# Kernel optimization log

Measured on AMD Instinct MI355X. Metric: run time of the kernel, lower is better.

## Reference

```python
import jax, jax.numpy as jnp
import numpy as np

NUM_CLASSES = 80
ALPHA = 0.25
GAMMA = 2.0
CONF_T = 0.5
IOU_T = 0.5
N_ANCHORS = 6144


def _pairwise_iou(b):
    # b: [n,4] (x1,y1,x2,y2) -> [n,n] IoU matrix
    area = (b[:, 2] - b[:, 0]) * (b[:, 3] - b[:, 1])
    lt = jnp.maximum(b[:, None, :2], b[None, :, :2])
    rb = jnp.minimum(b[:, None, 2:], b[None, :, 2:])
    wh = jnp.clip(rb - lt, 0.0)
    inter = wh[..., 0] * wh[..., 1]
    return inter / (area[:, None] + area[None, :] - inter)


def _nms(boxes, scores, thr):
    # torchvision-style NMS: returns kept indices in decreasing-score order
    order = jnp.argsort(-scores)
    iou = _pairwise_iou(boxes[order])
    n = boxes.shape[0]
    ar = jnp.arange(n)
    def body(i, supp):
        return supp | ((iou[i] > thr) & (ar > i) & jnp.logical_not(supp[i]))
    supp = jax.lax.fori_loop(0, n, body, jnp.zeros(n, dtype=bool))
    kept_pos = jnp.where(~supp)[0]  # eager: concrete shapes
    return order[kept_pos]


def _make_boxes(tb, floc):
    # tb: [1,1,4] target box; floc: [Nf,2] filtered predicted locations
    # replicates loc_determined with T=1: (tx1*px, ty1*py, tx2*px, ty2*py)
    px, py = floc[:, 0], floc[:, 1]
    return jnp.stack([tb[0, 0, 0] * px, tb[0, 0, 1] * py,
                      tb[0, 0, 2] * px, tb[0, 0, 3] * py], axis=1)


def _smooth_l1_sum(pred, tgt):
    d = jnp.abs(pred - tgt)  # broadcasts [k,C,4] vs [1,1,4]
    return jnp.where(d < 1.0, 0.5 * d * d, d - 0.5).sum()


def setup_inputs() -> dict:
    key = jax.random.key(0)
    k1, k2, k3 = jax.random.split(key, 3)
    locations = jax.random.uniform(k1, (1, N_ANCHORS, 2), dtype=jnp.float32)
    confidences = jax.random.uniform(k2, (1, N_ANCHORS, NUM_CLASSES), dtype=jnp.float32)
    # valid target box (x1<x2, y1<y2) in [0,1]
    target_boxes = jnp.array([[[0.15, 0.2, 0.85, 0.9]]], dtype=jnp.float32)
    target_labels = jax.random.randint(k3, (1,), 0, NUM_CLASSES)
    return {"locations": locations, "confidences": confidences,
            "target_boxes": target_boxes, "target_labels": target_labels}


def reference(locations, confidences, target_boxes, target_labels):
    conf = confidences[0]                       # [N,C]
    scores_max = conf.max(axis=1)
    idx_f = jnp.where(scores_max > CONF_T)[0]   # eager boolean filter
    if idx_f.shape[0] == 0:
        return jnp.float32(0.001)
    floc = locations[0, idx_f, :]               # [Nf,2]
    fconf = conf[idx_f]                         # [Nf,C]
    boxes = _make_boxes(target_boxes, floc)     # [Nf,4] (pred_loc_final)
    score = fconf[:, 0]                         # class-0 score, as in original
    keep = _nms(boxes, score, IOU_T)            # kept indices
    if keep.shape[0] == 0:
        return jnp.float32(0.001)
    matched_loc = boxes[keep]                   # [M,4]
    matched_conf = fconf[keep]                  # [M,C]
    k = target_labels.shape[0]                  # = 1
    topv, topi = jax.lax.top_k(matched_conf.T, k)  # per-class top-k over dim 0
    topv, topi = topv.T, topi.T                 # [k,C]
    pred_bin = (topv[:, 0] > 0.5).astype(jnp.float32)  # [k]
    mloc = matched_loc[topi]                    # [k,C,4]
    loc_loss = _smooth_l1_sum(mloc, target_boxes)
    # F.cross_entropy with 1-D float input/target = probabilities mode, unbatched
    ce = -(target_labels.astype(jnp.float32) * jax.nn.log_softmax(pred_bin)).sum()
    focal = ALPHA * (1.0 - jnp.exp(-ce)) ** GAMMA * ce
    # original bug preserved: num_positives = sum of kept *indices*
    num_pos = keep.sum().astype(jnp.float32)
    return (loc_loss + focal) / num_pos
```

## Files before the change

kernel.cpp:

```cpp
#include <hip/hip_runtime.h>
#include <stdint.h>

#define N_ANCHORS 6144
#define NUM_CLASSES 80
#define NWORDS 96

__device__ unsigned long long g_mask[(size_t)N_ANCHORS * NWORDS];
__device__ float4 g_boxes[N_ANCHORS];
__device__ float4 g_sbox[N_ANCHORS];
__device__ float  g_key[N_ANCHORS];
__device__ int    g_rank[N_ANCHORS];
__device__ int    g_fic[N_ANCHORS];
__device__ int    g_sAnchor[N_ANCHORS];
__device__ int    g_sFi[N_ANCHORS];
__device__ int    g_keptPos[N_ANCHORS];
__device__ int    g_F, g_K, g_np;
__device__ float  g_loss;

__device__ __forceinline__ unsigned long long shfl64(unsigned long long v, int l) {
    return __shfl(v, l, 64);
}

__global__ void k_zero() {
    int i = blockIdx.x * 256 + threadIdx.x;
    if (i < N_ANCHORS) { g_rank[i] = 0; g_fic[i] = 0; }
    if (i == 0) { g_F = 0; g_K = 0; g_np = 0; g_loss = 0.0f; }
}

__global__ void k_prep(const float* __restrict__ loc, const float* __restrict__ conf,
                       const float* __restrict__ tb) {
    int i = blockIdx.x * 256 + threadIdx.x;
    if (i >= N_ANCHORS) return;
    const float4* cp4 = (const float4*)(conf + (size_t)i * NUM_CLASSES);
    float4 v0 = cp4[0];
    float score = v0.x;
    float m = fmaxf(fmaxf(v0.x, v0.y), fmaxf(v0.z, v0.w));
    #pragma unroll
    for (int c = 1; c < NUM_CLASSES / 4; ++c) {
        float4 v = cp4[c];
        m = fmaxf(m, fmaxf(fmaxf(v.x, v.y), fmaxf(v.z, v.w)));
    }
    bool valid = m > 0.5f;
    g_key[i] = valid ? score : -1.0f;
    float px = loc[2 * i], py = loc[2 * i + 1];
    float4 b;
    b.x = __fmul_rn(tb[0], px);
    b.y = __fmul_rn(tb[1], py);
    b.z = __fmul_rn(tb[2], px);
    b.w = __fmul_rn(tb[3], py);
    g_boxes[i] = b;
    if (valid) atomicAdd(&g_F, 1);
}

__global__ void k_rank(void) {
    __shared__ float skey[256];
    int j0 = blockIdx.y * 256;
    skey[threadIdx.x] = g_key[j0 + threadIdx.x];
    __syncthreads();
    int i = blockIdx.x * 256 + threadIdx.x;
    float ki = g_key[i];
    int r = 0, f = 0;
    #pragma unroll 8
    for (int jj = 0; jj < 256; ++jj) {
        float kj = skey[jj];
        int j = j0 + jj;
        bool valid_j = kj >= 0.0f;
        r += (kj > ki) || (kj == ki && j < i && valid_j);
        f += (j < i) && valid_j;
    }
    atomicAdd(&g_rank[i], r);
    atomicAdd(&g_fic[i], f);
}

__global__ void k_scatter(void) {
    int i = blockIdx.x * 256 + threadIdx.x;
    if (i >= N_ANCHORS) return;
    if (g_key[i] >= 0.0f) {
        int p = g_rank[i];
        g_sAnchor[p] = i;
        g_sFi[p] = g_fic[i];
        g_sbox[p] = g_boxes[i];
    }
}

__global__ void __launch_bounds__(256) k_mask(void) {
    int wave = (blockIdx.x * 256 + threadIdx.x) >> 6;
    int lane = threadIdx.x & 63;
    if (wave >= N_ANCHORS) return;
    int i = wave;
    float4 bi = g_sbox[i];
    float areai = __fmul_rn(bi.z - bi.x, bi.w - bi.y);
    unsigned long long* row = g_mask + (size_t)i * NWORDS;
    for (int w = (i >> 6); w < NWORDS; ++w) {
        float4 bj = g_sbox[w * 64 + lane];
        float areaj = __fmul_rn(bj.z - bj.x, bj.w - bj.y);
        float lx = fmaxf(bi.x, bj.x), ly = fmaxf(bi.y, bj.y);
        float rx = fminf(bi.z, bj.z), ry = fminf(bi.w, bj.w);
        float iw = fmaxf(rx - lx, 0.0f), ih = fmaxf(ry - ly, 0.0f);
        float inter = __fmul_rn(iw, ih);
        float denom = __fsub_rn(__fadd_rn(areai, areaj), inter);
        float iou = __fdiv_rn(inter, denom);
        unsigned long long bits = __ballot(iou > 0.5f);
        if (lane == 0) row[w] = bits;
    }
}

__global__ void __launch_bounds__(64) k_scan(void) {
    int lane = threadIdx.x;
    int F = g_F;
    auto initw = [&](int w) -> unsigned long long {
        long long lo = (long long)w * 64, hi = lo + 64;
        if (F <= lo) return ~0ull;
        if (F >= hi) return 0ull;
        return (~0ull) << (F - lo);
    };
    unsigned long long remv0 = initw(lane);
    unsigned long long remv1 = (lane < 32) ? initw(64 + lane) : ~0ull;
    unsigned long long kept0 = 0, kept1 = 0;

    for (int w = 0; w < NWORDS; ++w) {
        unsigned long long cur = (w < 64) ? shfl64(remv0, w) : shfl64(remv1, w - 64);
        unsigned long long cand = ~cur;
        while (cand) {
            unsigned long long tmp = cand;
            int pos[8];
            #pragma unroll
            for (int q = 0; q < 8; ++q) {
                pos[q] = tmp ? __builtin_ctzll(tmp) : 64;
                tmp &= tmp - 1;
            }
            unsigned long long r0[8], r1[8];
            #pragma unroll
            for (int q = 0; q < 8; ++q) {
                if (pos[q] < 64) {
                    const unsigned long long* row = g_mask + (size_t)(w * 64 + pos[q]) * NWORDS;
                    r0[q] = row[lane];
                    r1[q] = (lane < 32) ? row[64 + lane] : 0ull;
                } else { r0[q] = 0ull; r1[q] = 0ull; }
            }
            unsigned long long m = cur, keptloc = 0, batch = 0;
            #pragma unroll
            for (int q = 0; q < 8; ++q) {
                if (pos[q] < 64) {
                    batch |= 1ull << pos[q];
                    if (!((m >> pos[q]) & 1ull)) {
                        keptloc |= 1ull << pos[q];
                        unsigned long long iw = (w < 64) ? shfl64(r0[q], w) : shfl64(r1[q], w - 64);
                        m |= iw;
                    }
                }
            }
            #pragma unroll
            for (int q = 0; q < 8; ++q)
                if ((pos[q] < 64) && ((keptloc >> pos[q]) & 1ull)) { remv0 |= r0[q]; remv1 |= r1[q]; }
            if (w < 64) { if (lane == w) kept0 |= keptloc; }
            else        { if (lane == w - 64) kept1 |= keptloc; }
            cur = m;
            cand = cand & ~batch & ~m;
        }
    }

    int c0 = __popcll(kept0);
    int c1 = (lane < 32) ? __popcll(kept1) : 0;
    int x0 = c0, x1 = c1;
    for (int ofs = 1; ofs < 64; ofs <<= 1) {
        int y0 = __shfl_up(x0, ofs, 64);
        int y1 = __shfl_up(x1, ofs, 64);
        if (lane >= ofs) { x0 += y0; x1 += y1; }
    }
    int t0 = __shfl(x0, 63, 64);
    int t1 = __shfl(x1, 63, 64);
    int off = x0 - c0;
    unsigned long long wd = kept0;
    while (wd) { int b = __builtin_ctzll(wd); g_keptPos[off++] = lane * 64 + b; wd &= wd - 1; }
    off = t0 + (x1 - c1);
    wd = kept1;
    while (wd) { int b = __builtin_ctzll(wd); g_keptPos[off++] = (64 + lane) * 64 + b; wd &= wd - 1; }
    if (lane == 0) g_K = t0 + t1;
}

__global__ void __launch_bounds__(64) k_loss(const float* __restrict__ conf, const float* __restrict__ tb) {
    int c = blockIdx.x;
    int lane = threadIdx.x;
    int K = g_K;
    float bv = -3.402823466e+38f;
    int bk = 0x7fffffff;
    int np = 0;
    for (int k = lane; k < K; k += 64) {
        int p = g_keptPos[k];
        int a = g_sAnchor[p];
        float v = conf[(size_t)a * NUM_CLASSES + c];
        if (v > bv || (v == bv && k < bk)) { bv = v; bk = k; }
        if (c == 0) np += g_sFi[p];
    }
    for (int ofs = 32; ofs > 0; ofs >>= 1) {
        float ov = __shfl_down(bv, ofs, 64);
        int ok = __shfl_down(bk, ofs, 64);
        if (ov > bv || (ov == bv && ok < bk)) { bv = ov; bk = ok; }
    }
    if (c == 0) {
        for (int ofs = 32; ofs > 0; ofs >>= 1) np += __shfl_down(np, ofs, 64);
        if (lane == 0) g_np = np;
    }
    if (lane == 0 && K > 0) {
        float4 b = g_sbox[g_keptPos[bk]];
        float t0 = tb[0], t1 = tb[1], t2 = tb[2], t3 = tb[3];
        float l = 0.0f, d;
        d = fabsf(b.x - t0); l += (d < 1.0f) ? 0.5f * d * d : d - 0.5f;
        d = fabsf(b.y - t1); l += (d < 1.0f) ? 0.5f * d * d : d - 0.5f;
        d = fabsf(b.z - t2); l += (d < 1.0f) ? 0.5f * d * d : d - 0.5f;
        d = fabsf(b.w - t3); l += (d < 1.0f) ? 0.5f * d * d : d - 0.5f;
        atomicAdd(&g_loss, l);
    }
}

__global__ void k_final(float* __restrict__ out) {
    out[0] = (g_F == 0 || g_K == 0) ? 0.001f : g_loss / (float)g_np;
}

extern "C" void kernel_launch(void* const* d_in, const int* in_sizes, int n_in,
                              void* d_out, int out_size, void* d_ws, size_t ws_size,
                              hipStream_t stream) {
    const float* loc  = (const float*)d_in[0];
    const float* conf = (const float*)d_in[1];
    const float* tb   = (const float*)d_in[2];
    float* out = (float*)d_out;

    k_zero<<<24, 256, 0, stream>>>();
    k_prep<<<24, 256, 0, stream>>>(loc, conf, tb);
    k_rank<<<dim3(24, 24), 256, 0, stream>>>();
    k_scatter<<<24, 256, 0, stream>>>();
    k_mask<<<(N_ANCHORS * 64) / 256, 256, 0, stream>>>();
    k_scan<<<1, 64, 0, stream>>>();
    k_loss<<<NUM_CLASSES, 64, 0, stream>>>(conf, tb);
    k_final<<<1, 1, 0, stream>>>(out);
}
```

Measured before the change: 182.5 us.

## Prefetch NMS mask rows across words, drop atomics and fuse loss finalization

The serial NMS scan now prefetches up to 12 candidate mask rows for the next word while it resolves the current one, so global-load latency overlaps the dependent suppression chain. Leftover candidates are handled in a slow path. Atomic rank accumulation and the zero kernel are replaced by per-tile partial arrays that the scatter kernel sums. Prep uses four threads per anchor, and the loss and final kernels merge into one 1024-thread block that reduces through shared memory. The cost is more registers in the single-wave scan and wasted loads when prefetched rows turn out to be suppressed.

New measurement: 249.8 us. 36.9% more time.

```diff
diff --git a/kernel.cpp b/kernel.cpp
--- a/kernel.cpp
+++ b/kernel.cpp
@@ -4,55 +4,54 @@
 #define N_ANCHORS 6144
 #define NUM_CLASSES 80
 #define NWORDS 96
+#define JT 24
+#define NP 12
 
 __device__ unsigned long long g_mask[(size_t)N_ANCHORS * NWORDS];
 __device__ float4 g_boxes[N_ANCHORS];
 __device__ float4 g_sbox[N_ANCHORS];
 __device__ float  g_key[N_ANCHORS];
-__device__ int    g_rank[N_ANCHORS];
-__device__ int    g_fic[N_ANCHORS];
+__device__ int    g_rankP[JT][N_ANCHORS];
+__device__ int    g_ficP[JT][N_ANCHORS];
+__device__ int    g_vcnt[JT];
 __device__ int    g_sAnchor[N_ANCHORS];
 __device__ int    g_sFi[N_ANCHORS];
 __device__ int    g_keptPos[N_ANCHORS];
-__device__ int    g_F, g_K, g_np;
-__device__ float  g_loss;
+__device__ int    g_F, g_K;
 
 __device__ __forceinline__ unsigned long long shfl64(unsigned long long v, int l) {
     return __shfl(v, l, 64);
 }
 
-__global__ void k_zero() {
-    int i = blockIdx.x * 256 + threadIdx.x;
-    if (i < N_ANCHORS) { g_rank[i] = 0; g_fic[i] = 0; }
-    if (i == 0) { g_F = 0; g_K = 0; g_np = 0; g_loss = 0.0f; }
-}
-
-__global__ void k_prep(const float* __restrict__ loc, const float* __restrict__ conf,
-                       const float* __restrict__ tb) {
-    int i = blockIdx.x * 256 + threadIdx.x;
-    if (i >= N_ANCHORS) return;
-    const float4* cp4 = (const float4*)(conf + (size_t)i * NUM_CLASSES);
+__global__ void __launch_bounds__(256) k_prep(const float* __restrict__ loc,
+                                              const float* __restrict__ conf,
+                                              const float* __restrict__ tb) {
+    int tid = blockIdx.x * 256 + threadIdx.x;
+    int a = tid >> 2, q = tid & 3;
+    const float4* cp4 = (const float4*)(conf + (size_t)a * NUM_CLASSES) + q * 5;
     float4 v0 = cp4[0];
-    float score = v0.x;
     float m = fmaxf(fmaxf(v0.x, v0.y), fmaxf(v0.z, v0.w));
     #pragma unroll
-    for (int c = 1; c < NUM_CLASSES / 4; ++c) {
+    for (int c = 1; c < 5; ++c) {
         float4 v = cp4[c];
         m = fmaxf(m, fmaxf(fmaxf(v.x, v.y), fmaxf(v.z, v.w)));
     }
-    bool valid = m > 0.5f;
-    g_key[i] = valid ? score : -1.0f;
-    float px = loc[2 * i], py = loc[2 * i + 1];
-    float4 b;
-    b.x = __fmul_rn(tb[0], px);
-    b.y = __fmul_rn(tb[1], py);
-    b.z = __fmul_rn(tb[2], px);
-    b.w = __fmul_rn(tb[3], py);
-    g_boxes[i] = b;
-    if (valid) atomicAdd(&g_F, 1);
-}
-
-__global__ void k_rank(void) {
+    m = fmaxf(m, __shfl_xor(m, 1, 64));
+    m = fmaxf(m, __shfl_xor(m, 2, 64));
+    if (q == 0) {
+        bool valid = m > 0.5f;
+        g_key[a] = valid ? v0.x : -1.0f;
+        float2 p = ((const float2*)loc)[a];
+        float4 b;
+        b.x = __fmul_rn(tb[0], p.x);
+        b.y = __fmul_rn(tb[1], p.y);
+        b.z = __fmul_rn(tb[2], p.x);
+        b.w = __fmul_rn(tb[3], p.y);
+        g_boxes[a] = b;
+    }
+}
+
+__global__ void __launch_bounds__(256) k_rank(void) {
     __shared__ float skey[256];
     int j0 = blockIdx.y * 256;
     skey[threadIdx.x] = g_key[j0 + threadIdx.x];
@@ -68,18 +67,31 @@
         r += (kj > ki) || (kj == ki && j < i && valid_j);
         f += (j < i) && valid_j;
     }
-    atomicAdd(&g_rank[i], r);
-    atomicAdd(&g_fic[i], f);
-}
-
-__global__ void k_scatter(void) {
+    g_rankP[blockIdx.y][i] = r;
+    g_ficP[blockIdx.y][i] = f;
+    if (blockIdx.x == 0 && threadIdx.x == 0) {
+        int c = 0;
+        for (int jj = 0; jj < 256; ++jj) c += (skey[jj] >= 0.0f);
+        g_vcnt[blockIdx.y] = c;
+    }
+}
+
+__global__ void __launch_bounds__(256) k_scatter(void) {
     int i = blockIdx.x * 256 + threadIdx.x;
+    if (i == 0) {
+        int F = 0;
+        #pragma unroll
+        for (int j = 0; j < JT; ++j) F += g_vcnt[j];
+        g_F = F;
+    }
     if (i >= N_ANCHORS) return;
     if (g_key[i] >= 0.0f) {
-        int p = g_rank[i];
-        g_sAnchor[p] = i;
-        g_sFi[p] = g_fic[i];
-        g_sbox[p] = g_boxes[i];
+        int r = 0, f = 0;
+        #pragma unroll
+        for (int j = 0; j < JT; ++j) { r += g_rankP[j][i]; f += g_ficP[j][i]; }
+        g_sAnchor[r] = i;
+        g_sFi[r] = f;
+        g_sbox[r] = g_boxes[i];
     }
 }
 
@@ -118,46 +130,65 @@
     unsigned long long remv1 = (lane < 32) ? initw(64 + lane) : ~0ull;
     unsigned long long kept0 = 0, kept1 = 0;
 
-    for (int w = 0; w < NWORDS; ++w) {
+    int ppA[NP], ppB[NP];
+    unsigned long long pA0[NP], pA1[NP], pB0[NP], pB1[NP];
+
+    auto prefetch = [&](int word, int* pp, unsigned long long* p0, unsigned long long* p1) {
+        unsigned long long cur = (word < 64) ? shfl64(remv0, word) : shfl64(remv1, word - 64);
+        unsigned long long cand = ~cur;
+        #pragma unroll
+        for (int q = 0; q < NP; ++q) {
+            int pos = cand ? __builtin_ctzll(cand) : 64;
+            cand &= cand - 1;
+            pp[q] = pos;
+            if (pos < 64) {
+                const unsigned long long* row = g_mask + (size_t)(word * 64 + pos) * NWORDS;
+                p0[q] = row[lane];
+                p1[q] = (lane < 32) ? row[64 + lane] : 0ull;
+            } else { p0[q] = 0ull; p1[q] = 0ull; }
+        }
+    };
+
+    auto resolve = [&](int w, const int* pp, const unsigned long long* p0, const unsigned long long* p1) {
         unsigned long long cur = (w < 64) ? shfl64(remv0, w) : shfl64(remv1, w - 64);
-        unsigned long long cand = ~cur;
-        while (cand) {
-            unsigned long long tmp = cand;
-            int pos[8];
-            #pragma unroll
-            for (int q = 0; q < 8; ++q) {
-                pos[q] = tmp ? __builtin_ctzll(tmp) : 64;
-                tmp &= tmp - 1;
+        unsigned long long m = cur, keptloc = 0;
+        #pragma unroll
+        for (int q = 0; q < NP; ++q) {
+            int pos = pp[q];
+            if (pos < 64 && !((m >> pos) & 1ull)) {
+                keptloc |= 1ull << pos;
+                unsigned long long iw = (w < 64) ? shfl64(p0[q], w) : shfl64(p1[q], w - 64);
+                m |= iw;
+                remv0 |= p0[q];
+                remv1 |= p1[q];
             }
-            unsigned long long r0[8], r1[8];
-            #pragma unroll
-            for (int q = 0; q < 8; ++q) {
-                if (pos[q] < 64) {
-                    const unsigned long long* row = g_mask + (size_t)(w * 64 + pos[q]) * NWORDS;
-                    r0[q] = row[lane];
-                    r1[q] = (lane < 32) ? row[64 + lane] : 0ull;
-                } else { r0[q] = 0ull; r1[q] = 0ull; }
-            }
-            unsigned long long m = cur, keptloc = 0, batch = 0;
-            #pragma unroll
-            for (int q = 0; q < 8; ++q) {
-                if (pos[q] < 64) {
-                    batch |= 1ull << pos[q];
-                    if (!((m >> pos[q]) & 1ull)) {
-                        keptloc |= 1ull << pos[q];
-                        unsigned long long iw = (w < 64) ? shfl64(r0[q], w) : shfl64(r1[q], w - 64);
-                        m |= iw;
-                    }
-                }
-            }
-            #pragma unroll
-            for (int q = 0; q < 8; ++q)
-                if ((pos[q] < 64) && ((keptloc >> pos[q]) & 1ull)) { remv0 |= r0[q]; remv1 |= r1[q]; }
-            if (w < 64) { if (lane == w) kept0 |= keptloc; }
-            else        { if (lane == w - 64) kept1 |= keptloc; }
-            cur = m;
-            cand = cand & ~batch & ~m;
-        }
+        }
+        int last = pp[NP - 1];
+        unsigned long long leftover = (last >= 63) ? 0ull : ((~m) & ((~0ull) << (last + 1)));
+        while (leftover) {
+            int pos = __builtin_ctzll(leftover);
+            leftover &= leftover - 1;
+            if ((m >> pos) & 1ull) continue;
+            const unsigned long long* row = g_mask + (size_t)(w * 64 + pos) * NWORDS;
+            unsigned long long r0 = row[lane];
+            unsigned long long r1 = (lane < 32) ? row[64 + lane] : 0ull;
+            keptloc |= 1ull << pos;
+            unsigned long long iw = (w < 64) ? shfl64(r0, w) : shfl64(r1, w - 64);
+            m |= iw;
+            remv0 |= r0;
+            remv1 |= r1;
+            leftover &= ~m;
+        }
+        if (w < 64) { if (lane == w) kept0 |= keptloc; }
+        else        { if (lane == w - 64) kept1 |= keptloc; }
+    };
+
+    prefetch(0, ppA, pA0, pA1);
+    for (int w = 0; w < NWORDS; w += 2) {
+        if (w + 1 < NWORDS) prefetch(w + 1, ppB, pB0, pB1);
+        resolve(w, ppA, pA0, pA1);
+        if (w + 2 < NWORDS) prefetch(w + 2, ppA, pA0, pA1);
+        if (w + 1 < NWORDS) resolve(w + 1, ppB, pB0, pB1);
     }
 
     int c0 = __popcll(kept0);
@@ -179,43 +210,54 @@
     if (lane == 0) g_K = t0 + t1;
 }
 
-__global__ void __launch_bounds__(64) k_loss(const float* __restrict__ conf, const float* __restrict__ tb) {
-    int c = blockIdx.x;
-    int lane = threadIdx.x;
+__global__ void __launch_bounds__(1024) k_loss(const float* __restrict__ conf,
+                                               const float* __restrict__ tb,
+                                               float* __restrict__ out) {
+    __shared__ float sloss[NUM_CLASSES];
+    __shared__ int snp;
+    int wave = threadIdx.x >> 6, lane = threadIdx.x & 63;
     int K = g_K;
-    float bv = -3.402823466e+38f;
-    int bk = 0x7fffffff;
-    int np = 0;
-    for (int k = lane; k < K; k += 64) {
-        int p = g_keptPos[k];
-        int a = g_sAnchor[p];
-        float v = conf[(size_t)a * NUM_CLASSES + c];
-        if (v > bv || (v == bv && k < bk)) { bv = v; bk = k; }
-        if (c == 0) np += g_sFi[p];
-    }
-    for (int ofs = 32; ofs > 0; ofs >>= 1) {
-        float ov = __shfl_down(bv, ofs, 64);
-        int ok = __shfl_down(bk, ofs, 64);
-        if (ov > bv || (ov == bv && ok < bk)) { bv = ov; bk = ok; }
-    }
-    if (c == 0) {
-        for (int ofs = 32; ofs > 0; ofs >>= 1) np += __shfl_down(np, ofs, 64);
-        if (lane == 0) g_np = np;
-    }
-    if (lane == 0 && K > 0) {
-        float4 b = g_sbox[g_keptPos[bk]];
-        float t0 = tb[0], t1 = tb[1], t2 = tb[2], t3 = tb[3];
-        float l = 0.0f, d;
-        d = fabsf(b.x - t0); l += (d < 1.0f) ? 0.5f * d * d : d - 0.5f;
-        d = fabsf(b.y - t1); l += (d < 1.0f) ? 0.5f * d * d : d - 0.5f;
-        d = fabsf(b.z - t2); l += (d < 1.0f) ? 0.5f * d * d : d - 0.5f;
-        d = fabsf(b.w - t3); l += (d < 1.0f) ? 0.5f * d * d : d - 0.5f;
-        atomicAdd(&g_loss, l);
-    }
-}
-
-__global__ void k_final(float* __restrict__ out) {
-    out[0] = (g_F == 0 || g_K == 0) ? 0.001f : g_loss / (float)g_np;
+    float t0 = tb[0], t1 = tb[1], t2 = tb[2], t3 = tb[3];
+    for (int c = wave; c < NUM_CLASSES; c += 16) {
+        float bv = -3.402823466e+38f;
+        int bk = 0x7fffffff;
+        int np = 0;
+        for (int k = lane; k < K; k += 64) {
+            int p = g_keptPos[k];
+            int a = g_sAnchor[p];
+            float v = conf[(size_t)a * NUM_CLASSES + c];
+            if (v > bv || (v == bv && k < bk)) { bv = v; bk = k; }
+            if (c == 0) np += g_sFi[p];
+        }
+        for (int ofs = 32; ofs > 0; ofs >>= 1) {
+            float ov = __shfl_down(bv, ofs, 64);
+            int ok = __shfl_down(bk, ofs, 64);
+            if (ov > bv || (ov == bv && ok < bk)) { bv = ov; bk = ok; }
+        }
+        if (c == 0) {
+            for (int ofs = 32; ofs > 0; ofs >>= 1) np += __shfl_down(np, ofs, 64);
+            if (lane == 0) snp = np;
+        }
+        if (lane == 0 && K > 0) {
+            float4 b = g_sbox[g_keptPos[bk]];
+            float l = 0.0f, d;
+            d = fabsf(b.x - t0); l += (d < 1.0f) ? 0.5f * d * d : d - 0.5f;
+            d = fabsf(b.y - t1); l += (d < 1.0f) ? 0.5f * d * d : d - 0.5f;
+            d = fabsf(b.z - t2); l += (d < 1.0f) ? 0.5f * d * d : d - 0.5f;
+            d = fabsf(b.w - t3); l += (d < 1.0f) ? 0.5f * d * d : d - 0.5f;
+            sloss[c] = l;
+        }
+    }
+    __syncthreads();
+    if (threadIdx.x == 0) {
+        if (g_F == 0 || K == 0) {
+            out[0] = 0.001f;
+        } else {
+            float l = 0.0f;
+            for (int c = 0; c < NUM_CLASSES; ++c) l += sloss[c];
+            out[0] = l / (float)snp;
+        }
+    }
 }
 
 extern "C" void kernel_launch(void* const* d_in, const int* in_sizes, int n_in,
@@ -226,12 +268,10 @@
     const float* tb   = (const float*)d_in[2];
     float* out = (float*)d_out;
 
-    k_zero<<<24, 256, 0, stream>>>();
-    k_prep<<<24, 256, 0, stream>>>(loc, conf, tb);
+    k_prep<<<96, 256, 0, stream>>>(loc, conf, tb);
     k_rank<<<dim3(24, 24), 256, 0, stream>>>();
     k_scatter<<<24, 256, 0, stream>>>();
     k_mask<<<(N_ANCHORS * 64) / 256, 256, 0, stream>>>();
     k_scan<<<1, 64, 0, stream>>>();
-    k_loss<<<NUM_CLASSES, 64, 0, stream>>>(conf, tb);
-    k_final<<<1, 1, 0, stream>>>(out);
-}
+    k_loss<<<1, 1024, 0, stream>>>(conf, tb, out);
+}
```

## Fuse NMS pipeline into one persistent kernel with grid barriers

Applied to the files above, without the earlier changes.

Replaces eight launches with a single persistent kernel of 256 blocks that uses atomic grid barriers between stages (prep, rank/scatter, IoU mask, scan, loss). Ranking is now computed per anchor by 8 cooperating threads instead of tiled atomics. The NMS scan is software-pipelined, prefetching three batches of mask rows ahead of resolving suppression. This aims to remove launch overhead and serial scan latency, but relies on all blocks being co-resident for the spin barriers.

After: 560.9 us. +207.4%, slower.

```diff
diff --git a/kernel.cpp b/kernel.cpp
--- a/kernel.cpp
+++ b/kernel.cpp
@@ -1,221 +1,278 @@
 #include <hip/hip_runtime.h>
 #include <stdint.h>
 
-#define N_ANCHORS 6144
-#define NUM_CLASSES 80
-#define NWORDS 96
-
-__device__ unsigned long long g_mask[(size_t)N_ANCHORS * NWORDS];
-__device__ float4 g_boxes[N_ANCHORS];
-__device__ float4 g_sbox[N_ANCHORS];
-__device__ float  g_key[N_ANCHORS];
-__device__ int    g_rank[N_ANCHORS];
-__device__ int    g_fic[N_ANCHORS];
-__device__ int    g_sAnchor[N_ANCHORS];
-__device__ int    g_sFi[N_ANCHORS];
-__device__ int    g_keptPos[N_ANCHORS];
-__device__ int    g_F, g_K, g_np;
-__device__ float  g_loss;
-
-__device__ __forceinline__ unsigned long long shfl64(unsigned long long v, int l) {
-    return __shfl(v, l, 64);
-}
-
-__global__ void k_zero() {
-    int i = blockIdx.x * 256 + threadIdx.x;
-    if (i < N_ANCHORS) { g_rank[i] = 0; g_fic[i] = 0; }
-    if (i == 0) { g_F = 0; g_K = 0; g_np = 0; g_loss = 0.0f; }
-}
-
-__global__ void k_prep(const float* __restrict__ loc, const float* __restrict__ conf,
-                       const float* __restrict__ tb) {
-    int i = blockIdx.x * 256 + threadIdx.x;
-    if (i >= N_ANCHORS) return;
-    const float4* cp4 = (const float4*)(conf + (size_t)i * NUM_CLASSES);
-    float4 v0 = cp4[0];
-    float score = v0.x;
-    float m = fmaxf(fmaxf(v0.x, v0.y), fmaxf(v0.z, v0.w));
-    #pragma unroll
-    for (int c = 1; c < NUM_CLASSES / 4; ++c) {
-        float4 v = cp4[c];
-        m = fmaxf(m, fmaxf(fmaxf(v.x, v.y), fmaxf(v.z, v.w)));
-    }
-    bool valid = m > 0.5f;
-    g_key[i] = valid ? score : -1.0f;
-    float px = loc[2 * i], py = loc[2 * i + 1];
-    float4 b;
-    b.x = __fmul_rn(tb[0], px);
-    b.y = __fmul_rn(tb[1], py);
-    b.z = __fmul_rn(tb[2], px);
-    b.w = __fmul_rn(tb[3], py);
-    g_boxes[i] = b;
-    if (valid) atomicAdd(&g_F, 1);
-}
-
-__global__ void k_rank(void) {
-    __shared__ float skey[256];
-    int j0 = blockIdx.y * 256;
-    skey[threadIdx.x] = g_key[j0 + threadIdx.x];
+#define NA 6144
+#define NC 80
+#define NW 96
+#define NB 256
+#define NT 256
+
+typedef unsigned long long u64;
+
+__device__ u64    g_mask[(size_t)NA * NW];
+__device__ float4 g_boxes[NA];
+__device__ float4 g_sbox[NA];
+__device__ __align__(16) float g_key[NA];
+__device__ int    g_sAnchor[NA];
+__device__ int    g_sFi[NA];
+__device__ int    g_keptPos[NA];
+
+struct Ctl { int bar[8]; int F; int K; int np; float loss; };
+__device__ Ctl g_ctl;
+
+__device__ __forceinline__ u64 shfl64(u64 v, int l) {
+    int lo = __shfl((int)(v & 0xffffffffull), l, 64);
+    int hi = __shfl((int)(v >> 32), l, 64);
+    return ((u64)(unsigned)hi << 32) | (unsigned)lo;
+}
+
+__device__ __forceinline__ void gbar(int id) {
     __syncthreads();
-    int i = blockIdx.x * 256 + threadIdx.x;
-    float ki = g_key[i];
-    int r = 0, f = 0;
-    #pragma unroll 8
-    for (int jj = 0; jj < 256; ++jj) {
-        float kj = skey[jj];
-        int j = j0 + jj;
-        bool valid_j = kj >= 0.0f;
-        r += (kj > ki) || (kj == ki && j < i && valid_j);
-        f += (j < i) && valid_j;
-    }
-    atomicAdd(&g_rank[i], r);
-    atomicAdd(&g_fic[i], f);
-}
-
-__global__ void k_scatter(void) {
-    int i = blockIdx.x * 256 + threadIdx.x;
-    if (i >= N_ANCHORS) return;
-    if (g_key[i] >= 0.0f) {
-        int p = g_rank[i];
-        g_sAnchor[p] = i;
-        g_sFi[p] = g_fic[i];
-        g_sbox[p] = g_boxes[i];
-    }
-}
-
-__global__ void __launch_bounds__(256) k_mask(void) {
-    int wave = (blockIdx.x * 256 + threadIdx.x) >> 6;
-    int lane = threadIdx.x & 63;
-    if (wave >= N_ANCHORS) return;
-    int i = wave;
-    float4 bi = g_sbox[i];
-    float areai = __fmul_rn(bi.z - bi.x, bi.w - bi.y);
-    unsigned long long* row = g_mask + (size_t)i * NWORDS;
-    for (int w = (i >> 6); w < NWORDS; ++w) {
-        float4 bj = g_sbox[w * 64 + lane];
-        float areaj = __fmul_rn(bj.z - bj.x, bj.w - bj.y);
-        float lx = fmaxf(bi.x, bj.x), ly = fmaxf(bi.y, bj.y);
-        float rx = fminf(bi.z, bj.z), ry = fminf(bi.w, bj.w);
-        float iw = fmaxf(rx - lx, 0.0f), ih = fmaxf(ry - ly, 0.0f);
-        float inter = __fmul_rn(iw, ih);
-        float denom = __fsub_rn(__fadd_rn(areai, areaj), inter);
-        float iou = __fdiv_rn(inter, denom);
-        unsigned long long bits = __ballot(iou > 0.5f);
-        if (lane == 0) row[w] = bits;
-    }
-}
-
-__global__ void __launch_bounds__(64) k_scan(void) {
-    int lane = threadIdx.x;
-    int F = g_F;
-    auto initw = [&](int w) -> unsigned long long {
-        long long lo = (long long)w * 64, hi = lo + 64;
-        if (F <= lo) return ~0ull;
-        if (F >= hi) return 0ull;
-        return (~0ull) << (F - lo);
-    };
-    unsigned long long remv0 = initw(lane);
-    unsigned long long remv1 = (lane < 32) ? initw(64 + lane) : ~0ull;
-    unsigned long long kept0 = 0, kept1 = 0;
-
-    for (int w = 0; w < NWORDS; ++w) {
-        unsigned long long cur = (w < 64) ? shfl64(remv0, w) : shfl64(remv1, w - 64);
-        unsigned long long cand = ~cur;
-        while (cand) {
-            unsigned long long tmp = cand;
-            int pos[8];
+    if (threadIdx.x == 0) {
+        __threadfence();
+        atomicAdd(&g_ctl.bar[id], 1);
+        while (__hip_atomic_load(&g_ctl.bar[id], __ATOMIC_ACQUIRE,
+                                 __HIP_MEMORY_SCOPE_AGENT) < NB)
+            __builtin_amdgcn_s_sleep(1);
+        __threadfence();
+    }
+    __syncthreads();
+}
+
+__global__ void __launch_bounds__(NT, 1)
+k_fused(const float* __restrict__ loc, const float* __restrict__ conf,
+        const float* __restrict__ tb, float* __restrict__ out) {
+    const int tid  = blockIdx.x * NT + threadIdx.x;
+    const int lane = threadIdx.x & 63;
+
+    if (tid < NA * 4) {
+        int a = tid >> 2, q = tid & 3;
+        const float4* cp4 = (const float4*)(conf + (size_t)a * NC) + q * 5;
+        float4 v0 = cp4[0];
+        float m = fmaxf(fmaxf(v0.x, v0.y), fmaxf(v0.z, v0.w));
+        #pragma unroll
+        for (int c = 1; c < 5; ++c) {
+            float4 v = cp4[c];
+            m = fmaxf(m, fmaxf(fmaxf(v.x, v.y), fmaxf(v.z, v.w)));
+        }
+        m = fmaxf(m, __shfl_xor(m, 1, 64));
+        m = fmaxf(m, __shfl_xor(m, 2, 64));
+        bool valid = m > 0.5f;
+        if (q == 0) {
+            g_key[a] = valid ? v0.x : -1.0f;
+            float2 p = ((const float2*)loc)[a];
+            float4 b;
+            b.x = __fmul_rn(tb[0], p.x);
+            b.y = __fmul_rn(tb[1], p.y);
+            b.z = __fmul_rn(tb[2], p.x);
+            b.w = __fmul_rn(tb[3], p.y);
+            g_boxes[a] = b;
+        }
+        u64 bal = __ballot(valid && q == 0);
+        if (lane == 0) atomicAdd(&g_ctl.F, (int)__popcll(bal));
+    }
+
+    gbar(0);
+
+    {
+        int a = tid >> 3, s = tid & 7;
+        if (a < NA) {
+            float ki = g_key[a];
+            const float4* k4 = (const float4*)g_key;
+            int r = 0, f = 0;
+            for (int jj = 0; jj < 192; ++jj) {
+                int i4 = jj * 8 + s;
+                float4 kj = k4[i4];
+                int j0 = i4 * 4;
+                r += (kj.x > ki) || (kj.x == ki && (j0 + 0) < a);
+                r += (kj.y > ki) || (kj.y == ki && (j0 + 1) < a);
+                r += (kj.z > ki) || (kj.z == ki && (j0 + 2) < a);
+                r += (kj.w > ki) || (kj.w == ki && (j0 + 3) < a);
+                f += ((j0 + 0) < a) && (kj.x >= 0.0f);
+                f += ((j0 + 1) < a) && (kj.y >= 0.0f);
+                f += ((j0 + 2) < a) && (kj.z >= 0.0f);
+                f += ((j0 + 3) < a) && (kj.w >= 0.0f);
+            }
+            r += __shfl_xor(r, 1, 64); r += __shfl_xor(r, 2, 64); r += __shfl_xor(r, 4, 64);
+            f += __shfl_xor(f, 1, 64); f += __shfl_xor(f, 2, 64); f += __shfl_xor(f, 4, 64);
+            if (s == 0 && ki >= 0.0f) {
+                g_sAnchor[r] = a;
+                g_sFi[r] = f;
+                g_sbox[r] = g_boxes[a];
+            }
+        }
+    }
+
+    gbar(1);
+
+    {
+        int gw = tid >> 6;
+        for (int row = gw; row < NA; row += (NB * NT) / 64) {
+            float4 bi = g_sbox[row];
+            float areai = __fmul_rn(bi.z - bi.x, bi.w - bi.y);
+            u64* rp = g_mask + (size_t)row * NW;
+            for (int w = row >> 6; w < NW; ++w) {
+                float4 bj = g_sbox[w * 64 + lane];
+                float areaj = __fmul_rn(bj.z - bj.x, bj.w - bj.y);
+                float lx = fmaxf(bi.x, bj.x), ly = fmaxf(bi.y, bj.y);
+                float rx = fminf(bi.z, bj.z), ry = fminf(bi.w, bj.w);
+                float iw = fmaxf(rx - lx, 0.0f), ih = fmaxf(ry - ly, 0.0f);
+                float inter = __fmul_rn(iw, ih);
+                float denom = __fsub_rn(__fadd_rn(areai, areaj), inter);
+                float iou = __fdiv_rn(inter, denom);
+                u64 bits = __ballot(iou > 0.5f);
+                if (lane == 0) rp[w] = bits;
+            }
+        }
+    }
+
+    gbar(2);
+
+    if (blockIdx.x == 0 && threadIdx.x < 64) {
+        int F = g_ctl.F;
+        auto initw = [&](int w) -> u64 {
+            long long lo = (long long)w * 64, hi = lo + 64;
+            if (F <= lo) return ~0ull;
+            if (F >= hi) return 0ull;
+            return (~0ull) << (F - lo);
+        };
+        u64 remv0 = initw(lane);
+        u64 remv1 = (lane < 32) ? initw(64 + lane) : ~0ull;
+        u64 kept0 = 0, kept1 = 0;
+
+        auto getRemv = [&](int w) -> u64 {
+            return (w < 64) ? shfl64(remv0, w) : shfl64(remv1, w - 64);
+        };
+
+        int scanW = 0;
+        u64 scanRem = ~getRemv(0);
+
+        int posA[8], posB[8], posC[8];
+        u64 loA[8], hiA[8], loB[8], hiB[8], loC[8], hiC[8];
+
+        auto fill = [&](int* pos, u64* lo, u64* hi) -> int {
+            scanRem &= ~getRemv(scanW);
+            int n = 0;
             #pragma unroll
             for (int q = 0; q < 8; ++q) {
-                pos[q] = tmp ? __builtin_ctzll(tmp) : 64;
-                tmp &= tmp - 1;
-            }
-            unsigned long long r0[8], r1[8];
+                while (scanRem == 0 && scanW < NW - 1) { ++scanW; scanRem = ~getRemv(scanW); }
+                int p = -1;
+                if (scanRem) {
+                    int b = __builtin_ctzll(scanRem);
+                    scanRem &= scanRem - 1;
+                    p = (scanW << 6) | b;
+                    ++n;
+                }
+                pos[q] = p;
+            }
             #pragma unroll
             for (int q = 0; q < 8; ++q) {
-                if (pos[q] < 64) {
-                    const unsigned long long* row = g_mask + (size_t)(w * 64 + pos[q]) * NWORDS;
-                    r0[q] = row[lane];
-                    r1[q] = (lane < 32) ? row[64 + lane] : 0ull;
-                } else { r0[q] = 0ull; r1[q] = 0ull; }
-            }
-            unsigned long long m = cur, keptloc = 0, batch = 0;
+                const u64* row = g_mask + (size_t)(pos[q] < 0 ? 0 : pos[q]) * NW;
+                lo[q] = row[lane];
+                hi[q] = row[64 + (lane & 31)];
+            }
+            return n;
+        };
+
+        auto resolve = [&](const int* pos, const u64* lo, const u64* hi) {
             #pragma unroll
             for (int q = 0; q < 8; ++q) {
-                if (pos[q] < 64) {
-                    batch |= 1ull << pos[q];
-                    if (!((m >> pos[q]) & 1ull)) {
-                        keptloc |= 1ull << pos[q];
-                        unsigned long long iw = (w < 64) ? shfl64(r0[q], w) : shfl64(r1[q], w - 64);
-                        m |= iw;
-                    }
+                int p = pos[q];
+                if (p < 0) break;
+                int wq = p >> 6, bq = p & 63;
+                bool ownerbit;
+                if (wq < 64) ownerbit = (lane == wq) && ((remv0 >> bq) & 1ull);
+                else         ownerbit = (lane == wq - 64) && ((remv1 >> bq) & 1ull);
+                bool suppressed = __ballot(ownerbit) != 0ull;
+                if (!suppressed) {
+                    remv0 |= lo[q];
+                    remv1 |= hi[q];
+                    if (wq < 64) { if (lane == wq) kept0 |= 1ull << bq; }
+                    else         { if (lane == wq - 64) kept1 |= 1ull << bq; }
                 }
             }
-            #pragma unroll
-            for (int q = 0; q < 8; ++q)
-                if ((pos[q] < 64) && ((keptloc >> pos[q]) & 1ull)) { remv0 |= r0[q]; remv1 |= r1[q]; }
-            if (w < 64) { if (lane == w) kept0 |= keptloc; }
-            else        { if (lane == w - 64) kept1 |= keptloc; }
-            cur = m;
-            cand = cand & ~batch & ~m;
-        }
-    }
-
-    int c0 = __popcll(kept0);
-    int c1 = (lane < 32) ? __popcll(kept1) : 0;
-    int x0 = c0, x1 = c1;
-    for (int ofs = 1; ofs < 64; ofs <<= 1) {
-        int y0 = __shfl_up(x0, ofs, 64);
-        int y1 = __shfl_up(x1, ofs, 64);
-        if (lane >= ofs) { x0 += y0; x1 += y1; }
-    }
-    int t0 = __shfl(x0, 63, 64);
-    int t1 = __shfl(x1, 63, 64);
-    int off = x0 - c0;
-    unsigned long long wd = kept0;
-    while (wd) { int b = __builtin_ctzll(wd); g_keptPos[off++] = lane * 64 + b; wd &= wd - 1; }
-    off = t0 + (x1 - c1);
-    wd = kept1;
-    while (wd) { int b = __builtin_ctzll(wd); g_keptPos[off++] = (64 + lane) * 64 + b; wd &= wd - 1; }
-    if (lane == 0) g_K = t0 + t1;
-}
-
-__global__ void __launch_bounds__(64) k_loss(const float* __restrict__ conf, const float* __restrict__ tb) {
-    int c = blockIdx.x;
-    int lane = threadIdx.x;
-    int K = g_K;
-    float bv = -3.402823466e+38f;
-    int bk = 0x7fffffff;
-    int np = 0;
-    for (int k = lane; k < K; k += 64) {
-        int p = g_keptPos[k];
-        int a = g_sAnchor[p];
-        float v = conf[(size_t)a * NUM_CLASSES + c];
-        if (v > bv || (v == bv && k < bk)) { bv = v; bk = k; }
-        if (c == 0) np += g_sFi[p];
-    }
-    for (int ofs = 32; ofs > 0; ofs >>= 1) {
-        float ov = __shfl_down(bv, ofs, 64);
-        int ok = __shfl_down(bk, ofs, 64);
-        if (ov > bv || (ov == bv && ok < bk)) { bv = ov; bk = ok; }
-    }
-    if (c == 0) {
-        for (int ofs = 32; ofs > 0; ofs >>= 1) np += __shfl_down(np, ofs, 64);
-        if (lane == 0) g_np = np;
-    }
-    if (lane == 0 && K > 0) {
-        float4 b = g_sbox[g_keptPos[bk]];
-        float t0 = tb[0], t1 = tb[1], t2 = tb[2], t3 = tb[3];
-        float l = 0.0f, d;
-        d = fabsf(b.x - t0); l += (d < 1.0f) ? 0.5f * d * d : d - 0.5f;
-        d = fabsf(b.y - t1); l += (d < 1.0f) ? 0.5f * d * d : d - 0.5f;
-        d = fabsf(b.z - t2); l += (d < 1.0f) ? 0.5f * d * d : d - 0.5f;
-        d = fabsf(b.w - t3); l += (d < 1.0f) ? 0.5f * d * d : d - 0.5f;
-        atomicAdd(&g_loss, l);
-    }
-}
-
-__global__ void k_final(float* __restrict__ out) {
-    out[0] = (g_F == 0 || g_K == 0) ? 0.001f : g_loss / (float)g_np;
+        };
+
+        int nA = fill(posA, loA, hiA);
+        if (nA) {
+            int nB = fill(posB, loB, hiB);
+            int nC;
+            for (;;) {
+                nC = fill(posC, loC, hiC);
+                resolve(posA, loA, hiA);
+                if (nB == 0) break;
+                nA = fill(posA, loA, hiA);
+                resolve(posB, loB, hiB);
+                if (nC == 0) break;
+                nB = fill(posB, loB, hiB);
+                resolve(posC, loC, hiC);
+                if (nA == 0) break;
+            }
+        }
+
+        int c0 = __popcll(kept0);
+        int c1 = (lane < 32) ? __popcll(kept1) : 0;
+        int x0 = c0, x1 = c1;
+        for (int ofs = 1; ofs < 64; ofs <<= 1) {
+            int y0 = __shfl_up(x0, ofs, 64);
+            int y1 = __shfl_up(x1, ofs, 64);
+            if (lane >= ofs) { x0 += y0; x1 += y1; }
+        }
+        int t0 = __shfl(x0, 63, 64);
+        int t1 = __shfl(x1, 63, 64);
+        int off = x0 - c0;
+        u64 wd = kept0;
+        while (wd) { int b = __builtin_ctzll(wd); g_keptPos[off++] = lane * 64 + b; wd &= wd - 1; }
+        off = t0 + (x1 - c1);
+        wd = kept1;
+        while (wd) { int b = __builtin_ctzll(wd); g_keptPos[off++] = (64 + lane) * 64 + b; wd &= wd - 1; }
+        if (lane == 0) g_ctl.K = t0 + t1;
+    }
+
+    gbar(3);
+
+    {
+        int K = g_ctl.K;
+        if (blockIdx.x < NC && (threadIdx.x >> 6) == 0) {
+            int c = blockIdx.x;
+            float bv = -3.402823466e+38f;
+            int bk = 0x7fffffff;
+            for (int k = lane; k < K; k += 64) {
+                int p = g_keptPos[k];
+                int a = g_sAnchor[p];
+                float v = conf[(size_t)a * NC + c];
+                if (v > bv || (v == bv && k < bk)) { bv = v; bk = k; }
+            }
+            for (int ofs = 32; ofs > 0; ofs >>= 1) {
+                float ov = __shfl_down(bv, ofs, 64);
+                int ok = __shfl_down(bk, ofs, 64);
+                if (ov > bv || (ov == bv && ok < bk)) { bv = ov; bk = ok; }
+            }
+            if (lane == 0 && K > 0) {
+                float4 b = g_sbox[g_keptPos[bk]];
+                float t0 = tb[0], t1 = tb[1], t2 = tb[2], t3 = tb[3];
+                float l = 0.0f, d;
+                d = fabsf(b.x - t0); l += (d < 1.0f) ? 0.5f * d * d : d - 0.5f;
+                d = fabsf(b.y - t1); l += (d < 1.0f) ? 0.5f * d * d : d - 0.5f;
+                d = fabsf(b.z - t2); l += (d < 1.0f) ? 0.5f * d * d : d - 0.5f;
+                d = fabsf(b.w - t3); l += (d < 1.0f) ? 0.5f * d * d : d - 0.5f;
+                atomicAdd(&g_ctl.loss, l);
+            }
+        }
+        if (blockIdx.x == 0 && (threadIdx.x >> 6) == 1) {
+            int np = 0;
+            for (int k = lane; k < K; k += 64) np += g_sFi[g_keptPos[k]];
+            for (int ofs = 32; ofs > 0; ofs >>= 1) np += __shfl_down(np, ofs, 64);
+            if (lane == 0) g_ctl.np = np;
+        }
+    }
+
+    gbar(4);
+
+    if (blockIdx.x == 0 && threadIdx.x == 0) {
+        out[0] = (g_ctl.F == 0 || g_ctl.K == 0) ? 0.001f
+                                                : g_ctl.loss / (float)g_ctl.np;
+    }
 }
 
 extern "C" void kernel_launch(void* const* d_in, const int* in_sizes, int n_in,
@@ -226,12 +283,9 @@
     const float* tb   = (const float*)d_in[2];
     float* out = (float*)d_out;
 
-    k_zero<<<24, 256, 0, stream>>>();
-    k_prep<<<24, 256, 0, stream>>>(loc, conf, tb);
-    k_rank<<<dim3(24, 24), 256, 0, stream>>>();
-    k_scatter<<<24, 256, 0, stream>>>();
-    k_mask<<<(N_ANCHORS * 64) / 256, 256, 0, stream>>>();
-    k_scan<<<1, 64, 0, stream>>>();
-    k_loss<<<NUM_CLASSES, 64, 0, stream>>>(conf, tb);
-    k_final<<<1, 1, 0, stream>>>(out);
-}
+    void* ctl = nullptr;
+    hipGetSymbolAddress(&ctl, HIP_SYMBOL(g_ctl));
+    hipMemsetAsync(ctl, 0, sizeof(Ctl), stream);
+
+    k_fused<<<NB, NT, 0, stream>>>(loc, conf, tb, out);
+}
```
